# Performance work log

Measured on AMD Instinct MI355X. Metric: run time of the kernel, lower is better.

Reference implementation:

```python
import jax, jax.numpy as jnp
import numpy as np

N_NODES = 50000
N_EDGES = 800000


def setup_inputs() -> dict:
    key = jax.random.key(0)
    ks = jax.random.split(key, 12)
    x = jax.random.normal(ks[0], (N_NODES, 500), dtype=jnp.float32)
    edge_src = jax.random.randint(ks[1], (N_EDGES,), 0, N_NODES, dtype=jnp.int32)
    edge_dst = jax.random.randint(ks[2], (N_EDGES,), 0, N_NODES, dtype=jnp.int32)
    edge_vals = jax.random.uniform(ks[3], (N_EDGES,), dtype=jnp.float32) * 0.1
    def w(k, fan_in, fan_out):
        s = 1.0 / np.sqrt(fan_in)
        return jax.random.uniform(k, (fan_in, fan_out), dtype=jnp.float32, minval=-s, maxval=s)
    W1 = w(ks[4], 500, 128)
    b1 = jnp.zeros((128,), jnp.float32)
    W2 = w(ks[5], 128, 64)
    b2 = jnp.zeros((64,), jnp.float32)
    W3 = w(ks[6], 64, 16)
    b3 = jnp.zeros((16,), jnp.float32)
    We = w(ks[7], 64, 64)
    be = jnp.zeros((64,), jnp.float32)
    return {"x": x, "edge_vals": edge_vals, "W1": W1, "b1": b1, "W2": W2,
            "b2": b2, "W3": W3, "b3": b3, "We": We, "be": be,
            "edge_src": edge_src, "edge_dst": edge_dst}


def reference(x, edge_vals, W1, b1, W2, b2, W3, b3, We, be, edge_src, edge_dst):
    n = x.shape[0]

    def gcn_layer(h, W, b):
        # GraphConvolution: support = h @ W ; out = spmm(adj, support) + b
        support = h @ W                                   # [N, d_out]
        msg = support[edge_dst] * edge_vals[:, None]      # [E, d_out]
        agg = jax.ops.segment_sum(msg, edge_src, num_segments=n)
        return agg + b

    h = jax.nn.relu(gcn_layer(x, W1, b1))
    # dropout omitted (eval mode, training=False)
    h = jax.nn.relu(gcn_layer(h, W2, b2))
    out1 = jax.nn.log_softmax(gcn_layer(h, W3, b3), axis=1)
    out2 = h @ We + be
    return (out1, out2)
```

## Files before the change

### kernel.cpp

```cpp
#include <hip/hip_runtime.h>
#include <hip/hip_bf16.h>
#include <math.h>

#define N_NODES 50000
#define N_EDGES 800000

typedef __attribute__((ext_vector_type(8))) short bf16x8;
typedef __attribute__((ext_vector_type(4))) float f32x4;

__device__ inline unsigned short f2bf(float f) {
    unsigned u = __float_as_uint(f);
    unsigned r = (u + 0x7fffu + ((u >> 16) & 1u)) >> 16;
    return (unsigned short)r;
}

__device__ inline bf16x8 pack8(float4 a0, float4 a1) {
    union { __hip_bfloat162 h2[4]; bf16x8 v; } u;
    u.h2[0] = __float22bfloat162_rn(make_float2(a0.x, a0.y));
    u.h2[1] = __float22bfloat162_rn(make_float2(a0.z, a0.w));
    u.h2[2] = __float22bfloat162_rn(make_float2(a1.x, a1.y));
    u.h2[3] = __float22bfloat162_rn(make_float2(a1.z, a1.w));
    return u.v;
}

__global__ __launch_bounds__(256) void convert_hist_kernel(
    const float* __restrict__ W1, const float* __restrict__ W2,
    const float* __restrict__ We, const float* __restrict__ W3,
    unsigned short* __restrict__ W1frag, unsigned short* __restrict__ W2frag,
    unsigned short* __restrict__ Wcfrag,
    const int* __restrict__ src, int* __restrict__ counts)
{
    if (blockIdx.x < 308) {
        int t = blockIdx.x * 256 + threadIdx.x;
        if (t < 65536) {
            int h = t >> 15;
            int r1 = t & 32767;
            int j = r1 >> 13;
            int r2 = r1 & 8191;
            int s = r2 >> 9;
            int r3 = r2 & 511;
            int lane = r3 >> 3, jj = r3 & 7;
            int k = s * 32 + (lane >> 4) * 8 + jj;
            int n = h * 64 + j * 16 + (lane & 15);
            float v = (k < 500) ? W1[k * 128 + n] : 0.0f;
            W1frag[t] = f2bf(v);
        } else if (t < 73728) {
            int t2 = t - 65536;
            int j = t2 >> 11;
            int s = (t2 >> 9) & 3;
            int lane = (t2 >> 3) & 63, jj = t2 & 7;
            int k = s * 32 + (lane >> 4) * 8 + jj;
            int n = j * 16 + (lane & 15);
            W2frag[t2] = f2bf(W2[k * 64 + n]);
        } else {
            int t3 = t - 73728;
            int j = t3 >> 10;
            int s = (t3 >> 9) & 1;
            int lane = (t3 >> 3) & 63, jj = t3 & 7;
            int k = s * 32 + (lane >> 4) * 8 + jj;
            int n = j * 16 + (lane & 15);
            float v = (n < 64) ? We[k * 64 + n] : W3[k * 16 + (n - 64)];
            Wcfrag[t3] = f2bf(v);
        }
    } else {
        int e = (blockIdx.x - 308) * 256 + threadIdx.x;
        if (e < N_EDGES) atomicAdd(&counts[src[e]], 1);
    }
}

__global__ __launch_bounds__(1024) void scan_kernel(
    const int* __restrict__ counts, int* __restrict__ row_ptr,
    int* __restrict__ cursor)
{
    constexpr int Q = N_NODES / 4;
    const int t = threadIdx.x;
    const int lane = t & 63, wave = t >> 6;
    __shared__ int wsum[16];
    __shared__ int carry_s;
    int carry = 0;
    const int4* c4 = reinterpret_cast<const int4*>(counts);
    int4* rp4 = reinterpret_cast<int4*>(row_ptr);
    int4* cu4 = reinterpret_cast<int4*>(cursor);

    for (int base = 0; base < Q; base += 4096) {
        int4 v[4];
        int ls[5];
        ls[0] = 0;
#pragma unroll
        for (int k = 0; k < 4; ++k) {
            const int g = base + t * 4 + k;
            if (g < Q) v[k] = c4[g];
            else       v[k] = make_int4(0, 0, 0, 0);
            ls[k + 1] = ls[k] + v[k].x + v[k].y + v[k].z + v[k].w;
        }
        const int s = ls[4];

        int incl = s;
#pragma unroll
        for (int off = 1; off < 64; off <<= 1) {
            int n = __shfl_up(incl, off, 64);
            if (lane >= off) incl += n;
        }
        if (lane == 63) wsum[wave] = incl;
        __syncthreads();
        if (t < 16) {
            int w = wsum[t];
            int inc = w;
#pragma unroll
            for (int off = 1; off < 16; off <<= 1) {
                int n = __shfl_up(inc, off, 64);
                if (t >= off) inc += n;
            }
            wsum[t] = inc - w;
            if (t == 15) carry_s = inc;
        }
        __syncthreads();
        const int e0 = carry + wsum[wave] + (incl - s);
#pragma unroll
        for (int k = 0; k < 4; ++k) {
            const int g = base + t * 4 + k;
            if (g < Q) {
                const int b0 = e0 + ls[k];
                int4 r;
                r.x = b0;
                r.y = r.x + v[k].x;
                r.z = r.y + v[k].y;
                r.w = r.z + v[k].z;
                rp4[g] = r;
                cu4[g] = r;
            }
        }
        carry += carry_s;
        __syncthreads();
    }
    if (t == 0) row_ptr[N_NODES] = carry;
}

__global__ __launch_bounds__(256) void fill_kernel(
    const int* __restrict__ src, const int* __restrict__ dst,
    const float* __restrict__ vals, int* __restrict__ cursor,
    int2* __restrict__ pairs)
{
    int e = blockIdx.x * 256 + threadIdx.x;
    if (e >= N_EDGES) return;
    int pos = atomicAdd(&cursor[src[e]], 1);
    pairs[pos] = make_int2(dst[e], __float_as_int(vals[e]));
}

__global__ __launch_bounds__(256, 2) void gemm1_mfma_kernel(
    const float* __restrict__ A,
    const unsigned short* __restrict__ W1frag,
    unsigned short* __restrict__ C)
{
    __shared__ __align__(16) unsigned short Bs[32768];

    const int t = threadIdx.x;
    const int h  = blockIdx.x & 1;
    const int br = blockIdx.x >> 1;
    const int lane = t & 63;
    const int wave = t >> 6;
    const int r = lane & 15, q = lane >> 4;

    {
        const uint4* src = reinterpret_cast<const uint4*>(W1frag + h * 32768);
        uint4* dst = reinterpret_cast<uint4*>(Bs);
#pragma unroll
        for (int i = 0; i < 16; ++i)
            dst[t + i * 256] = src[t + i * 256];
    }
    __syncthreads();

    const int col0 = h * 64;

    for (int c = br * 4 + wave; c < 3125; c += 1024) {
        const float* ap = A + (size_t)(c * 16 + r) * 500;

        f32x4 acc[4];
#pragma unroll
        for (int j = 0; j < 4; ++j) acc[j] = {0.f, 0.f, 0.f, 0.f};

#pragma unroll 4
        for (int s = 0; s < 16; ++s) {
            const int kb = s * 32 + q * 8;
            const int k0 = kb < 496 ? kb : 496;
            const int k1 = (kb + 4) < 496 ? (kb + 4) : 496;
            float4 a0 = *reinterpret_cast<const float4*>(ap + k0);
            float4 a1 = *reinterpret_cast<const float4*>(ap + k1);
            bf16x8 af = pack8(a0, a1);
#pragma unroll
            for (int j = 0; j < 4; ++j) {
                bf16x8 b = *reinterpret_cast<const bf16x8*>(
                    &Bs[(size_t)((j * 16 + s) * 64 + lane) * 8]);
                acc[j] = __builtin_amdgcn_mfma_f32_16x16x32_bf16(af, b, acc[j], 0, 0, 0);
            }
        }

#pragma unroll
        for (int reg = 0; reg < 4; ++reg) {
            const int grow = c * 16 + q * 4 + reg;
#pragma unroll
            for (int j = 0; j < 4; ++j)
                C[(size_t)grow * 128 + col0 + j * 16 + r] = f2bf(acc[j][reg]);
        }
    }
}

__global__ __launch_bounds__(256) void gather128_gemm2_kernel(
    const unsigned short* __restrict__ support, const int2* __restrict__ pairs,
    const int* __restrict__ row_ptr, const float* __restrict__ b1,
    const unsigned short* __restrict__ W2frag,
    unsigned short* __restrict__ sup2)
{
    __shared__ __align__(16) unsigned short Bs[8192];
    __shared__ __align__(16) unsigned short h1s[16 * 136];

    const int t = threadIdx.x;
    const int lane = t & 63, wave = t >> 6;
    const int f = lane & 15, e = lane >> 4;

    {
        const uint4* src = reinterpret_cast<const uint4*>(W2frag);
        uint4* dst = reinterpret_cast<uint4*>(Bs);
#pragma unroll
        for (int i = 0; i < 4; ++i)
            dst[t + i * 256] = src[t + i * 256];
    }

    const float4 ba = *reinterpret_cast<const float4*>(b1 + f * 8);
    const float4 bb = *reinterpret_cast<const float4*>(b1 + f * 8 + 4);
    const float bias[8] = {ba.x, ba.y, ba.z, ba.w, bb.x, bb.y, bb.z, bb.w};

    const int node0 = blockIdx.x * 16 + wave * 4;

    for (int nn = 0; nn < 4; ++nn) {
        const int node = node0 + nn;
        int i = row_ptr[node] + e;
        const int end = row_ptr[node + 1];

        float acc[8] = {};
        for (; i + 4 < end; i += 8) {
            int2 p0 = pairs[i], p1 = pairs[i + 4];
            float v0 = __int_as_float(p0.y), v1 = __int_as_float(p1.y);
            uint4 r0 = *reinterpret_cast<const uint4*>(support + (size_t)p0.x * 128 + f * 8);
            uint4 r1 = *reinterpret_cast<const uint4*>(support + (size_t)p1.x * 128 + f * 8);
            unsigned w0[4] = {r0.x, r0.y, r0.z, r0.w};
            unsigned w1[4] = {r1.x, r1.y, r1.z, r1.w};
#pragma unroll
            for (int j = 0; j < 4; ++j) {
                acc[2 * j]     += __uint_as_float(w0[j] << 16) * v0;
                acc[2 * j + 1] += __uint_as_float(w0[j] & 0xffff0000u) * v0;
                acc[2 * j]     += __uint_as_float(w1[j] << 16) * v1;
                acc[2 * j + 1] += __uint_as_float(w1[j] & 0xffff0000u) * v1;
            }
        }
        if (i < end) {
            int2 p = pairs[i];
            float v = __int_as_float(p.y);
            uint4 r = *reinterpret_cast<const uint4*>(support + (size_t)p.x * 128 + f * 8);
            unsigned w[4] = {r.x, r.y, r.z, r.w};
#pragma unroll
            for (int j = 0; j < 4; ++j) {
                acc[2 * j]     += __uint_as_float(w[j] << 16) * v;
                acc[2 * j + 1] += __uint_as_float(w[j] & 0xffff0000u) * v;
            }
        }
#pragma unroll
        for (int j = 0; j < 8; ++j) {
            acc[j] += __shfl_xor(acc[j], 16, 64);
            acc[j] += __shfl_xor(acc[j], 32, 64);
        }
        if (e == 0) {
            unsigned short hv[8];
#pragma unroll
            for (int j = 0; j < 8; ++j) {
                float v = acc[j] + bias[j];
                hv[j] = f2bf(v > 0.0f ? v : 0.0f);
            }
            *reinterpret_cast<uint4*>(&h1s[(wave * 4 + nn) * 136 + f * 8]) =
                *reinterpret_cast<uint4*>(hv);
        }
    }
    __syncthreads();

    f32x4 acc2 = {0.f, 0.f, 0.f, 0.f};
#pragma unroll
    for (int s = 0; s < 4; ++s) {
        bf16x8 af = *reinterpret_cast<const bf16x8*>(&h1s[f * 136 + (s * 4 + e) * 8]);
        bf16x8 b = *reinterpret_cast<const bf16x8*>(
            &Bs[(size_t)((wave * 4 + s) * 64 + lane) * 8]);
        acc2 = __builtin_amdgcn_mfma_f32_16x16x32_bf16(af, b, acc2, 0, 0, 0);
    }
#pragma unroll
    for (int reg = 0; reg < 4; ++reg) {
        const int grow = blockIdx.x * 16 + e * 4 + reg;
        sup2[(size_t)grow * 64 + wave * 16 + f] = f2bf(acc2[reg]);
    }
}

__global__ __launch_bounds__(256) void gemm3_mfma_kernel(
    const unsigned short* __restrict__ A,
    const unsigned short* __restrict__ Wcfrag,
    const float* __restrict__ be,
    float* __restrict__ out2,
    float* __restrict__ sup3)
{
    __shared__ __align__(16) unsigned short Bs[5120];

    const int t = threadIdx.x;
    const int lane = t & 63, wave = t >> 6;
    const int r = lane & 15, q = lane >> 4;

    {
        const uint4* src = reinterpret_cast<const uint4*>(Wcfrag);
        uint4* dst = reinterpret_cast<uint4*>(Bs);
#pragma unroll
        for (int i = 0; i < 2; ++i)
            dst[t + i * 256] = src[t + i * 256];
        if (t < 128) dst[512 + t] = src[512 + t];
    }
    __syncthreads();

    const int c = blockIdx.x * 4 + wave;
    if (c >= 3125) return;
    const unsigned short* ap = A + (size_t)(c * 16 + r) * 64 + q * 8;

    f32x4 acc[5];
#pragma unroll
    for (int j = 0; j < 5; ++j) acc[j] = {0.f, 0.f, 0.f, 0.f};

#pragma unroll
    for (int s = 0; s < 2; ++s) {
        bf16x8 af = *reinterpret_cast<const bf16x8*>(ap + s * 32);
#pragma unroll
        for (int j = 0; j < 5; ++j) {
            bf16x8 b = *reinterpret_cast<const bf16x8*>(
                &Bs[(size_t)((j * 2 + s) * 64 + lane) * 8]);
            acc[j] = __builtin_amdgcn_mfma_f32_16x16x32_bf16(af, b, acc[j], 0, 0, 0);
        }
    }

    float bev[4];
#pragma unroll
    for (int j = 0; j < 4; ++j) bev[j] = be[j * 16 + r];

#pragma unroll
    for (int reg = 0; reg < 4; ++reg) {
        const int grow = c * 16 + q * 4 + reg;
#pragma unroll
        for (int j = 0; j < 4; ++j)
            out2[(size_t)grow * 64 + j * 16 + r] = acc[j][reg] + bev[j];
        sup3[(size_t)grow * 16 + r] = acc[4][reg];
    }
}

__global__ __launch_bounds__(256) void gather64_kernel(
    const unsigned short* __restrict__ support, const int2* __restrict__ pairs,
    const int* __restrict__ row_ptr, const float* __restrict__ b2,
    unsigned short* __restrict__ h2)
{
    const int node = blockIdx.x * 4 + (threadIdx.x >> 6);
    const int lane = threadIdx.x & 63;
    const int f = lane & 7, e = lane >> 3;
    int i = row_ptr[node] + e;
    const int end = row_ptr[node + 1];

    float acc[8] = {};
    for (; i + 8 < end; i += 16) {
        int2 p0 = pairs[i], p1 = pairs[i + 8];
        float v0 = __int_as_float(p0.y), v1 = __int_as_float(p1.y);
        uint4 r0 = *reinterpret_cast<const uint4*>(support + (size_t)p0.x * 64 + f * 8);
        uint4 r1 = *reinterpret_cast<const uint4*>(support + (size_t)p1.x * 64 + f * 8);
        unsigned w0[4] = {r0.x, r0.y, r0.z, r0.w};
        unsigned w1[4] = {r1.x, r1.y, r1.z, r1.w};
#pragma unroll
        for (int j = 0; j < 4; ++j) {
            acc[2 * j]     += __uint_as_float(w0[j] << 16) * v0;
            acc[2 * j + 1] += __uint_as_float(w0[j] & 0xffff0000u) * v0;
            acc[2 * j]     += __uint_as_float(w1[j] << 16) * v1;
            acc[2 * j + 1] += __uint_as_float(w1[j] & 0xffff0000u) * v1;
        }
    }
    if (i < end) {
        int2 p = pairs[i];
        float v = __int_as_float(p.y);
        uint4 r = *reinterpret_cast<const uint4*>(support + (size_t)p.x * 64 + f * 8);
        unsigned w[4] = {r.x, r.y, r.z, r.w};
#pragma unroll
        for (int j = 0; j < 4; ++j) {
            acc[2 * j]     += __uint_as_float(w[j] << 16) * v;
            acc[2 * j + 1] += __uint_as_float(w[j] & 0xffff0000u) * v;
        }
    }
#pragma unroll
    for (int j = 0; j < 8; ++j) {
        acc[j] += __shfl_xor(acc[j], 8, 64);
        acc[j] += __shfl_xor(acc[j], 16, 64);
        acc[j] += __shfl_xor(acc[j], 32, 64);
    }
    if (e == 0) {
        const float4 ba = *reinterpret_cast<const float4*>(b2 + f * 8);
        const float4 bb = *reinterpret_cast<const float4*>(b2 + f * 8 + 4);
        float bias[8] = {ba.x, ba.y, ba.z, ba.w, bb.x, bb.y, bb.z, bb.w};
        unsigned short h[8];
#pragma unroll
        for (int j = 0; j < 8; ++j) {
            float v = acc[j] + bias[j];
            h[j] = f2bf(v > 0.0f ? v : 0.0f);
        }
        *reinterpret_cast<uint4*>(h2 + (size_t)node * 64 + f * 8) =
            *reinterpret_cast<uint4*>(h);
    }
}

__global__ __launch_bounds__(256) void gather16_lsm_kernel(
    const float* __restrict__ sup3, const int2* __restrict__ pairs,
    const int* __restrict__ row_ptr, const float* __restrict__ b3,
    float* __restrict__ out1)
{
    const int node = blockIdx.x * 4 + (threadIdx.x >> 6);
    const int lane = threadIdx.x & 63;
    const int f = lane & 3, e = lane >> 2;
    int i = row_ptr[node] + e;
    const int end = row_ptr[node + 1];

    float4 acc = {0, 0, 0, 0};
    for (; i + 16 < end; i += 32) {
        int2 p0 = pairs[i], p1 = pairs[i + 16];
        float v0 = __int_as_float(p0.y), v1 = __int_as_float(p1.y);
        float4 m0 = *reinterpret_cast<const float4*>(sup3 + (size_t)p0.x * 16 + f * 4);
        float4 m1 = *reinterpret_cast<const float4*>(sup3 + (size_t)p1.x * 16 + f * 4);
        acc.x += m0.x * v0 + m1.x * v1;
        acc.y += m0.y * v0 + m1.y * v1;
        acc.z += m0.z * v0 + m1.z * v1;
        acc.w += m0.w * v0 + m1.w * v1;
    }
    if (i < end) {
        int2 p = pairs[i];
        float v = __int_as_float(p.y);
        float4 m = *reinterpret_cast<const float4*>(sup3 + (size_t)p.x * 16 + f * 4);
        acc.x += m.x * v; acc.y += m.y * v; acc.z += m.z * v; acc.w += m.w * v;
    }
#pragma unroll
    for (int off = 4; off < 64; off <<= 1) {
        acc.x += __shfl_xor(acc.x, off, 64);
        acc.y += __shfl_xor(acc.y, off, 64);
        acc.z += __shfl_xor(acc.z, off, 64);
        acc.w += __shfl_xor(acc.w, off, 64);
    }
    const float4 b = *reinterpret_cast<const float4*>(b3 + f * 4);
    float a0 = acc.x + b.x, a1 = acc.y + b.y, a2 = acc.z + b.z, a3 = acc.w + b.w;
    float mx = fmaxf(fmaxf(a0, a1), fmaxf(a2, a3));
    mx = fmaxf(mx, __shfl_xor(mx, 1, 64));
    mx = fmaxf(mx, __shfl_xor(mx, 2, 64));
    float s = expf(a0 - mx) + expf(a1 - mx) + expf(a2 - mx) + expf(a3 - mx);
    s += __shfl_xor(s, 1, 64);
    s += __shfl_xor(s, 2, 64);
    const float lse = mx + logf(s);
    if (e == 0) {
        float4 o = {a0 - lse, a1 - lse, a2 - lse, a3 - lse};
        *reinterpret_cast<float4*>(out1 + (size_t)node * 16 + f * 4) = o;
    }
}

extern "C" void kernel_launch(void* const* d_in, const int* in_sizes, int n_in,
                              void* d_out, int out_size, void* d_ws, size_t ws_size,
                              hipStream_t stream)
{
    const float* x         = (const float*)d_in[0];
    const float* edge_vals = (const float*)d_in[1];
    const float* W1 = (const float*)d_in[2];
    const float* b1 = (const float*)d_in[3];
    const float* W2 = (const float*)d_in[4];
    const float* b2 = (const float*)d_in[5];
    const float* W3 = (const float*)d_in[6];
    const float* b3 = (const float*)d_in[7];
    const float* We = (const float*)d_in[8];
    const float* be = (const float*)d_in[9];
    const int* esrc = (const int*)d_in[10];
    const int* edst = (const int*)d_in[11];

    float* out1 = (float*)d_out;
    float* out2 = (float*)d_out + (size_t)N_NODES * 16;

    char* ws = (char*)d_ws;
    float* bufA    = (float*)(ws);
    float* bufB    = (float*)(ws + 25600000);
    float* bufC    = (float*)(ws + 51200000);
    int*   counts  = (int*)  (ws + 54400000);
    int*   row_ptr = (int*)  (ws + 54600064);
    int*   cursor  = (int*)  (ws + 54800128);
    int2*  pairs   = (int2*) (ws + 55000192);

    unsigned short* W1frag = (unsigned short*)bufC;
    unsigned short* W2frag = (unsigned short*)((char*)bufC + 131072);
    unsigned short* Wcfrag = (unsigned short*)((char*)bufC + 147456);

    unsigned short* sup1bf = (unsigned short*)bufA;
    unsigned short* sup2bf = (unsigned short*)bufB;
    unsigned short* h2bf   = (unsigned short*)bufA;
    float*          sup3   = (float*)((char*)bufB + 6400000);

    const int EB  = (N_EDGES + 255) / 256;
    const int GN  = N_NODES / 4;
    const int GB  = N_NODES / 16;
    const int G3  = 782;

    hipMemsetAsync(counts, 0, (size_t)N_NODES * 4, stream);
    convert_hist_kernel<<<308 + EB, 256, 0, stream>>>(
        W1, W2, We, W3, W1frag, W2frag, Wcfrag, esrc, counts);
    scan_kernel<<<1, 1024, 0, stream>>>(counts, row_ptr, cursor);
    fill_kernel<<<EB, 256, 0, stream>>>(esrc, edst, edge_vals, cursor, pairs);

    gemm1_mfma_kernel<<<512, 256, 0, stream>>>(x, W1frag, sup1bf);

    gather128_gemm2_kernel<<<GB, 256, 0, stream>>>(
        sup1bf, pairs, row_ptr, b1, W2frag, sup2bf);

    gather64_kernel<<<GN, 256, 0, stream>>>(sup2bf, pairs, row_ptr, b2, h2bf);

    gemm3_mfma_kernel<<<G3, 256, 0, stream>>>(h2bf, Wcfrag, be, out2, sup3);

    gather16_lsm_kernel<<<GN, 256, 0, stream>>>(sup3, pairs, row_ptr, b3, out1);
}
```

Measured before the change: 365.3 us.

## Fuse layer-2 gather with layer-3/edge GEMM through shared memory

Merges the 64-wide neighbor aggregation kernel with the following MFMA GEMM. Each block aggregates 16 nodes into an LDS tile of bf16 h2, then computes out2 and sup3 directly from LDS. This removes the global write and reread of h2 and one kernel launch. In exchange, each wave now processes four nodes serially, so there is less parallelism per node, and the block count drops by four times for the gather phase.

Result: no change. 358.9 us (-1.8%).

```diff
diff --git a/kernel.cpp b/kernel.cpp
--- a/kernel.cpp
+++ b/kernel.cpp
@@ -297,18 +297,18 @@
     }
 }
 
-__global__ __launch_bounds__(256) void gemm3_mfma_kernel(
-    const unsigned short* __restrict__ A,
-    const unsigned short* __restrict__ Wcfrag,
-    const float* __restrict__ be,
-    float* __restrict__ out2,
-    float* __restrict__ sup3)
+__global__ __launch_bounds__(256) void gather64_gemm3_kernel(
+    const unsigned short* __restrict__ support, const int2* __restrict__ pairs,
+    const int* __restrict__ row_ptr, const float* __restrict__ b2,
+    const unsigned short* __restrict__ Wcfrag, const float* __restrict__ be,
+    float* __restrict__ out2, float* __restrict__ sup3)
 {
     __shared__ __align__(16) unsigned short Bs[5120];
+    __shared__ __align__(16) unsigned short h2s[16 * 68];
 
     const int t = threadIdx.x;
     const int lane = t & 63, wave = t >> 6;
-    const int r = lane & 15, q = lane >> 4;
+    const int f = lane & 7, e = lane >> 3;
 
     {
         const uint4* src = reinterpret_cast<const uint4*>(Wcfrag);
@@ -318,97 +318,95 @@
             dst[t + i * 256] = src[t + i * 256];
         if (t < 128) dst[512 + t] = src[512 + t];
     }
+
+    const float4 ba = *reinterpret_cast<const float4*>(b2 + f * 8);
+    const float4 bb = *reinterpret_cast<const float4*>(b2 + f * 8 + 4);
+    const float bias[8] = {ba.x, ba.y, ba.z, ba.w, bb.x, bb.y, bb.z, bb.w};
+
+    const int node0 = blockIdx.x * 16 + wave * 4;
+
+    for (int nn = 0; nn < 4; ++nn) {
+        const int node = node0 + nn;
+        int i = row_ptr[node] + e;
+        const int end = row_ptr[node + 1];
+
+        float acc[8] = {};
+        for (; i + 8 < end; i += 16) {
+            int2 p0 = pairs[i], p1 = pairs[i + 8];
+            float v0 = __int_as_float(p0.y), v1 = __int_as_float(p1.y);
+            uint4 r0 = *reinterpret_cast<const uint4*>(support + (size_t)p0.x * 64 + f * 8);
+            uint4 r1 = *reinterpret_cast<const uint4*>(support + (size_t)p1.x * 64 + f * 8);
+            unsigned w0[4] = {r0.x, r0.y, r0.z, r0.w};
+            unsigned w1[4] = {r1.x, r1.y, r1.z, r1.w};
+#pragma unroll
+            for (int j = 0; j < 4; ++j) {
+                acc[2 * j]     += __uint_as_float(w0[j] << 16) * v0;
+                acc[2 * j + 1] += __uint_as_float(w0[j] & 0xffff0000u) * v0;
+                acc[2 * j]     += __uint_as_float(w1[j] << 16) * v1;
+                acc[2 * j + 1] += __uint_as_float(w1[j] & 0xffff0000u) * v1;
+            }
+        }
+        if (i < end) {
+            int2 p = pairs[i];
+            float v = __int_as_float(p.y);
+            uint4 r = *reinterpret_cast<const uint4*>(support + (size_t)p.x * 64 + f * 8);
+            unsigned w[4] = {r.x, r.y, r.z, r.w};
+#pragma unroll
+            for (int j = 0; j < 4; ++j) {
+                acc[2 * j]     += __uint_as_float(w[j] << 16) * v;
+                acc[2 * j + 1] += __uint_as_float(w[j] & 0xffff0000u) * v;
+            }
+        }
+#pragma unroll
+        for (int j = 0; j < 8; ++j) {
+            acc[j] += __shfl_xor(acc[j], 8, 64);
+            acc[j] += __shfl_xor(acc[j], 16, 64);
+            acc[j] += __shfl_xor(acc[j], 32, 64);
+        }
+        if (e == 0) {
+            unsigned short hv[8];
+#pragma unroll
+            for (int j = 0; j < 8; ++j) {
+                float v = acc[j] + bias[j];
+                hv[j] = f2bf(v > 0.0f ? v : 0.0f);
+            }
+            *reinterpret_cast<uint4*>(&h2s[(wave * 4 + nn) * 68 + f * 8]) =
+                *reinterpret_cast<uint4*>(hv);
+        }
+    }
     __syncthreads();
 
-    const int c = blockIdx.x * 4 + wave;
-    if (c >= 3125) return;
-    const unsigned short* ap = A + (size_t)(c * 16 + r) * 64 + q * 8;
-
-    f32x4 acc[5];
-#pragma unroll
-    for (int j = 0; j < 5; ++j) acc[j] = {0.f, 0.f, 0.f, 0.f};
-
-#pragma unroll
-    for (int s = 0; s < 2; ++s) {
-        bf16x8 af = *reinterpret_cast<const bf16x8*>(ap + s * 32);
-#pragma unroll
-        for (int j = 0; j < 5; ++j) {
-            bf16x8 b = *reinterpret_cast<const bf16x8*>(
-                &Bs[(size_t)((j * 2 + s) * 64 + lane) * 8]);
-            acc[j] = __builtin_amdgcn_mfma_f32_16x16x32_bf16(af, b, acc[j], 0, 0, 0);
-        }
-    }
-
-    float bev[4];
-#pragma unroll
-    for (int j = 0; j < 4; ++j) bev[j] = be[j * 16 + r];
-
+    const int r = lane & 15, q = lane >> 4;
+    const bf16x8 af0 = *reinterpret_cast<const bf16x8*>(&h2s[r * 68 + q * 8]);
+    const bf16x8 af1 = *reinterpret_cast<const bf16x8*>(&h2s[r * 68 + (4 + q) * 8]);
+
+    f32x4 accA = {0.f, 0.f, 0.f, 0.f};
+    accA = __builtin_amdgcn_mfma_f32_16x16x32_bf16(
+        af0, *reinterpret_cast<const bf16x8*>(&Bs[(size_t)((wave * 2 + 0) * 64 + lane) * 8]),
+        accA, 0, 0, 0);
+    accA = __builtin_amdgcn_mfma_f32_16x16x32_bf16(
+        af1, *reinterpret_cast<const bf16x8*>(&Bs[(size_t)((wave * 2 + 1) * 64 + lane) * 8]),
+        accA, 0, 0, 0);
+    const float bev = be[wave * 16 + r];
 #pragma unroll
     for (int reg = 0; reg < 4; ++reg) {
-        const int grow = c * 16 + q * 4 + reg;
-#pragma unroll
-        for (int j = 0; j < 4; ++j)
-            out2[(size_t)grow * 64 + j * 16 + r] = acc[j][reg] + bev[j];
-        sup3[(size_t)grow * 16 + r] = acc[4][reg];
-    }
-}
-
-__global__ __launch_bounds__(256) void gather64_kernel(
-    const unsigned short* __restrict__ support, const int2* __restrict__ pairs,
-    const int* __restrict__ row_ptr, const float* __restrict__ b2,
-    unsigned short* __restrict__ h2)
-{
-    const int node = blockIdx.x * 4 + (threadIdx.x >> 6);
-    const int lane = threadIdx.x & 63;
-    const int f = lane & 7, e = lane >> 3;
-    int i = row_ptr[node] + e;
-    const int end = row_ptr[node + 1];
-
-    float acc[8] = {};
-    for (; i + 8 < end; i += 16) {
-        int2 p0 = pairs[i], p1 = pairs[i + 8];
-        float v0 = __int_as_float(p0.y), v1 = __int_as_float(p1.y);
-        uint4 r0 = *reinterpret_cast<const uint4*>(support + (size_t)p0.x * 64 + f * 8);
-        uint4 r1 = *reinterpret_cast<const uint4*>(support + (size_t)p1.x * 64 + f * 8);
-        unsigned w0[4] = {r0.x, r0.y, r0.z, r0.w};
-        unsigned w1[4] = {r1.x, r1.y, r1.z, r1.w};
-#pragma unroll
-        for (int j = 0; j < 4; ++j) {
-            acc[2 * j]     += __uint_as_float(w0[j] << 16) * v0;
-            acc[2 * j + 1] += __uint_as_float(w0[j] & 0xffff0000u) * v0;
-            acc[2 * j]     += __uint_as_float(w1[j] << 16) * v1;
-            acc[2 * j + 1] += __uint_as_float(w1[j] & 0xffff0000u) * v1;
-        }
-    }
-    if (i < end) {
-        int2 p = pairs[i];
-        float v = __int_as_float(p.y);
-        uint4 r = *reinterpret_cast<const uint4*>(support + (size_t)p.x * 64 + f * 8);
-        unsigned w[4] = {r.x, r.y, r.z, r.w};
-#pragma unroll
-        for (int j = 0; j < 4; ++j) {
-            acc[2 * j]     += __uint_as_float(w[j] << 16) * v;
-            acc[2 * j + 1] += __uint_as_float(w[j] & 0xffff0000u) * v;
-        }
-    }
-#pragma unroll
-    for (int j = 0; j < 8; ++j) {
-        acc[j] += __shfl_xor(acc[j], 8, 64);
-        acc[j] += __shfl_xor(acc[j], 16, 64);
-        acc[j] += __shfl_xor(acc[j], 32, 64);
-    }
-    if (e == 0) {
-        const float4 ba = *reinterpret_cast<const float4*>(b2 + f * 8);
-        const float4 bb = *reinterpret_cast<const float4*>(b2 + f * 8 + 4);
-        float bias[8] = {ba.x, ba.y, ba.z, ba.w, bb.x, bb.y, bb.z, bb.w};
-        unsigned short h[8];
-#pragma unroll
-        for (int j = 0; j < 8; ++j) {
-            float v = acc[j] + bias[j];
-            h[j] = f2bf(v > 0.0f ? v : 0.0f);
-        }
-        *reinterpret_cast<uint4*>(h2 + (size_t)node * 64 + f * 8) =
-            *reinterpret_cast<uint4*>(h);
+        const int grow = blockIdx.x * 16 + q * 4 + reg;
+        out2[(size_t)grow * 64 + wave * 16 + r] = accA[reg] + bev;
+    }
+
+    if (wave == 0) {
+        f32x4 accB = {0.f, 0.f, 0.f, 0.f};
+        accB = __builtin_amdgcn_mfma_f32_16x16x32_bf16(
+            af0, *reinterpret_cast<const bf16x8*>(&Bs[(size_t)((4 * 2 + 0) * 64 + lane) * 8]),
+            accB, 0, 0, 0);
+        accB = __builtin_amdgcn_mfma_f32_16x16x32_bf16(
+            af1, *reinterpret_cast<const bf16x8*>(&Bs[(size_t)((4 * 2 + 1) * 64 + lane) * 8]),
+            accB, 0, 0, 0);
+#pragma unroll
+        for (int reg = 0; reg < 4; ++reg) {
+            const int grow = blockIdx.x * 16 + q * 4 + reg;
+            sup3[(size_t)grow * 16 + r] = accB[reg];
+        }
     }
 }
 
@@ -497,13 +495,11 @@
 
     unsigned short* sup1bf = (unsigned short*)bufA;
     unsigned short* sup2bf = (unsigned short*)bufB;
-    unsigned short* h2bf   = (unsigned short*)bufA;
-    float*          sup3   = (float*)((char*)bufB + 6400000);
+    float*          sup3   = bufA;
 
     const int EB  = (N_EDGES + 255) / 256;
     const int GN  = N_NODES / 4;
     const int GB  = N_NODES / 16;
-    const int G3  = 782;
 
     hipMemsetAsync(counts, 0, (size_t)N_NODES * 4, stream);
     convert_hist_kernel<<<308 + EB, 256, 0, stream>>>(
@@ -516,9 +512,8 @@
     gather128_gemm2_kernel<<<GB, 256, 0, stream>>>(
         sup1bf, pairs, row_ptr, b1, W2frag, sup2bf);
 
-    gather64_kernel<<<GN, 256, 0, stream>>>(sup2bf, pairs, row_ptr, b2, h2bf);
-
-    gemm3_mfma_kernel<<<G3, 256, 0, stream>>>(h2bf, Wcfrag, be, out2, sup3);
+    gather64_gemm3_kernel<<<GB, 256, 0, stream>>>(
+        sup2bf, pairs, row_ptr, b2, Wcfrag, be, out2, sup3);
 
     gather16_lsm_kernel<<<GN, 256, 0, stream>>>(sup3, pairs, row_ptr, b3, out1);
 }
```
